# Optimization experiments

Hardware: AMD Instinct MI355X
Metric: run time of the kernel (lower is better)

Reference implementation:

```python
import jax, jax.numpy as jnp
import numpy as np

NEG = -9.0e15


def setup_inputs() -> dict:
    key = jax.random.key(0)
    k_x, k_w, k_e, k_b, k_m = jax.random.split(key, 5)
    B, N, C, F = 2048, 64, 256, 256
    x = jax.random.normal(k_x, (B, N, C), dtype=jnp.float32)
    W = jax.random.normal(k_w, (2, C, F), dtype=jnp.float32) * (1.414 / np.sqrt(C + F))
    # full logit tensor; only entries where mask holds are ever read (equivalent
    # to torch's flat `e` scattered into the nonzero positions of adj)
    e = jax.random.normal(k_e, (F, N, N), dtype=jnp.float32)
    bias = jax.random.normal(k_b, (F,), dtype=jnp.float32) * (1.0 / np.sqrt(C))
    # symmetric adjacency mask with self-loops, density ~0.3
    m = jax.random.bernoulli(k_m, 0.3, (N, N))
    mask = (m | m.T) | jnp.eye(N, dtype=bool)
    return {"x": x, "W": W, "e": e, "bias": bias, "mask": mask}


def reference(x, W, e, bias, mask):
    # x: [B,N,C], W: [2,C,F], e: [F,N,N], bias: [F], mask: [N,N] bool
    h0 = x @ W[0]                                   # [B,N,F] (self term)
    h1 = x @ W[1]                                   # [B,N,F] (neighbor term)
    logits = jnp.where(mask[None, :, :], e, NEG)    # [F,N,N]
    adj = jax.nn.softmax(logits, axis=2)            # per-channel row softmax
    N = mask.shape[0]
    eye = jnp.eye(N, dtype=bool)
    d = jnp.diagonal(adj, axis1=1, axis2=2)         # [F,N]  (adj * E diagonal)
    off = jnp.where(eye[None, :, :], 0.0, adj)      # [F,N,N] (adj * (1-E))
    # (adj*E) @ h0 reduces to per-node diagonal scaling; off-diag is a
    # per-channel NxN matmul batched over B.
    out = d.T[None, :, :] * h0 + jnp.einsum('fnm,bmf->bnf', off, h1)
    return out + bias[None, None, :]
```

## Files before the change

kernel.cpp:

```cpp
#include <hip/hip_runtime.h>
#include <hip/hip_bf16.h>


typedef __attribute__((ext_vector_type(8))) short  fragA;
typedef __attribute__((ext_vector_type(4))) float  f32x4;
typedef __attribute__((ext_vector_type(8))) unsigned short u16x8;
typedef __attribute__((ext_vector_type(4))) unsigned short u16x4;

constexpr long OFF_OFF = 0;
constexpr long OFF_WT  = 2l * 1024 * 1024;
constexpr long OFF_DS  = OFF_WT + 512l * 256 * 2;
constexpr long OFF_XB  = OFF_DS + 64l * 256 * 4;
constexpr long OFF_G0  = OFF_XB + 131072l * 256 * 2;
constexpr long OFF_H1T = OFF_G0 + 131072l * 256 * 2;
constexpr long WS_NEED = OFF_H1T + 131072l * 256 * 2;

static __device__ inline unsigned short f2bf(float f) {
  __hip_bfloat16 h = __float2bfloat16(f);
  return __builtin_bit_cast(unsigned short, h);
}
static __device__ inline float bf2f(unsigned short u) {
  unsigned int x = ((unsigned int)u) << 16;
  return __builtin_bit_cast(float, x);
}
static __device__ __forceinline__ void gl16(const void* g, void* l) {
  __builtin_amdgcn_global_load_lds(
      (const __attribute__((address_space(1))) unsigned int*)g,
      (__attribute__((address_space(3))) unsigned int*)l, 16, 0, 0);
}
static __device__ __forceinline__ f32x4 mfma16(fragA a, fragA b, f32x4 c) {
  return __builtin_amdgcn_mfma_f32_16x16x32_bf16(a, b, c, 0, 0, 0);
}

__global__ __launch_bounds__(256) void k_pre(const float* __restrict__ x,
                                             const float* __restrict__ e,
                                             const float* __restrict__ W,
                                             const unsigned char* __restrict__ mask,
                                             char* __restrict__ ws_b) {
  const int bid = blockIdx.x;
  const int tid = threadIdx.x;
  if (bid < 4096) {
    unsigned short* off = (unsigned short*)(ws_b + OFF_OFF);
    float* dscale = (float*)(ws_b + OFF_DS);
    const int lane = tid & 63;
    const int row  = bid * 4 + (tid >> 6);
    const int n = row & 63;
    bool is_u8 = __all(mask[lane * 65] != 0);
    bool mv;
    if (is_u8) mv = mask[n * 64 + lane] != 0;
    else       mv = ((const int*)mask)[n * 64 + lane] != 0;
    float v = mv ? e[(long)row * 64 + lane] : -1e30f;
    float mx = v;
#pragma unroll
    for (int s = 32; s; s >>= 1) mx = fmaxf(mx, __shfl_xor(mx, s));
    float ex = mv ? __expf(v - mx) : 0.f;
    float sm = ex;
#pragma unroll
    for (int s = 32; s; s >>= 1) sm += __shfl_xor(sm, s);
    float adj = ex / sm;
    const int f = row >> 6;
    if (lane == n) dscale[n * 256 + f] = adj;
    off[(long)row * 64 + lane] = f2bf(lane == n ? 0.f : adj);
  } else if (bid < 6144) {
    unsigned short* xb = (unsigned short*)(ws_b + OFF_XB);
    long i = ((long)(bid - 4096) * 256 + tid) * 8;
    const long stride = 2048l * 256 * 8;
    const long total = 131072l * 256;
    for (; i < total; i += stride) {
      float4 a = *(const float4*)(x + i);
      float4 b = *(const float4*)(x + i + 4);
      u16x8 p;
      p[0] = f2bf(a.x); p[1] = f2bf(a.y); p[2] = f2bf(a.z); p[3] = f2bf(a.w);
      p[4] = f2bf(b.x); p[5] = f2bf(b.y); p[6] = f2bf(b.z); p[7] = f2bf(b.w);
      *(u16x8*)(xb + i) = p;
    }
  } else {
    unsigned short* Wt = (unsigned short*)(ws_b + OFF_WT);
    __shared__ float t[64][65];
    const int b2 = bid - 6144;
    const int w = b2 >> 4, f0 = ((b2 >> 2) & 3) * 64, c0 = (b2 & 3) * 64;
    const int tr = tid >> 2, tc = (tid & 3) * 16;
    const float* src = W + ((long)(w * 256 + c0 + tr)) * 256 + f0 + tc;
#pragma unroll
    for (int i = 0; i < 16; i += 4) {
      float4 v = *(const float4*)(src + i);
      t[tr][tc + i] = v.x; t[tr][tc + i + 1] = v.y;
      t[tr][tc + i + 2] = v.z; t[tr][tc + i + 3] = v.w;
    }
    __syncthreads();
    u16x8 p0, p1;
#pragma unroll
    for (int i = 0; i < 8; i++)  p0[i] = f2bf(t[tc + i][tr]);
#pragma unroll
    for (int i = 0; i < 8; i++)  p1[i] = f2bf(t[tc + 8 + i][tr]);
    unsigned short* dst = Wt + ((long)(w * 256 + f0 + tr)) * 256 + c0 + tc;
    *(u16x8*)dst = p0;
    *(u16x8*)(dst + 8) = p1;
  }
}

__global__ __launch_bounds__(256) void k_gemm(char* __restrict__ ws_b) {
  const float* dscale = (const float*)(ws_b + OFF_DS);
  const char* xb_b = ws_b + OFF_XB;
  const char* wt_b = ws_b + OFF_WT;
  unsigned short* g0g = (unsigned short*)(ws_b + OFF_G0);
  unsigned short* h1t = (unsigned short*)(ws_b + OFF_H1T);

  __shared__ __align__(16) char arena[65536];

  const int tid = threadIdx.x;
  const int wid = tid >> 6, lane = tid & 63;
  const int lr = lane & 15, qu = lane >> 4;

  const int wg = blockIdx.x;
  const int xcd = wg & 7, s = wg >> 3;
  const int rg = xcd * 128 + (s >> 3);
  const int cg = s & 7;
  const int f0 = cg * 32;
  const long R0 = (long)rg * 128;

  {
    const int c  = tid >> 5;
    const int cb = (tid & 31) * 16;
    const int sw = cb ^ ((c & 7) << 4);
#pragma unroll
    for (int i = 0; i < 8; i++) {
      int col  = i * 8 + c;
      int wrow = (col < 32) ? (f0 + col) : (224 + f0 + col);
      gl16(wt_b + (long)wrow * 512 + sw, arena + i * 4096 + tid * 16);
    }
  }
  const int ar = tid >> 3;
  const int aswz = ((tid & 7) ^ (ar & 7)) << 4;
#pragma unroll
  for (int i = 0; i < 4; i++)
    gl16(xb_b + (R0 + i * 32 + ar) * 512 + aswz, arena + 32768 + i * 4096 + tid * 16);

  f32x4 acc[2][4] = {};
  const int arow0 = wid * 32;

  for (int ks = 0; ks < 4; ks++) {
    __syncthreads();
    if (ks < 3) {
      const char* gsrc = xb_b + (ks + 1) * 128;
      char* ldst = arena + 32768 + ((ks + 1) & 1) * 16384;
#pragma unroll
      for (int i = 0; i < 4; i++)
        gl16(gsrc + (R0 + i * 32 + ar) * 512 + aswz, ldst + i * 4096 + tid * 16);
    }
    const char* ab = arena + 32768 + (ks & 1) * 16384;
    fragA af[2][2], bfr[2][4];
#pragma unroll
    for (int kk = 0; kk < 2; kk++) {
#pragma unroll
      for (int i2 = 0; i2 < 2; i2++) {
        int r = arow0 + i2 * 16 + lr;
        af[kk][i2] = *(const fragA*)(ab + r * 128 +
                        ((kk * 64 + qu * 16) ^ ((lr & 7) << 4)));
      }
#pragma unroll
      for (int j = 0; j < 4; j++) {
        int cc = j * 16 + lr;
        bfr[kk][j] = *(const fragA*)(arena + cc * 512 +
                        ((ks * 128 + kk * 64 + qu * 16) ^ ((lr & 7) << 4)));
      }
    }
#pragma unroll
    for (int kk = 0; kk < 2; kk++)
#pragma unroll
      for (int i2 = 0; i2 < 2; i2++)
#pragma unroll
        for (int j = 0; j < 4; j++)
          acc[i2][j] = mfma16(af[kk][i2], bfr[kk][j], acc[i2][j]);
  }
  __syncthreads();

  unsigned short* Gs = (unsigned short*)(arena + 32768);
  unsigned short* Ts = (unsigned short*)(arena + 49152);
#pragma unroll
  for (int i2 = 0; i2 < 2; i2++) {
#pragma unroll
    for (int j = 0; j < 2; j++) {
      int f = f0 + j * 16 + lr;
#pragma unroll
      for (int r = 0; r < 4; r++) {
        int rloc = arow0 + i2 * 16 + qu * 4 + r;
        int n = rloc & 63;
        Gs[rloc * 40 + j * 16 + lr] = f2bf(dscale[n * 256 + f] * acc[i2][j][r]);
      }
    }
#pragma unroll
    for (int j = 2; j < 4; j++) {
      int fl = (j - 2) * 16 + lr;
      int rb = arow0 + i2 * 16 + qu * 4;
      u16x4 pk;
      pk[0] = f2bf(acc[i2][j][0]); pk[1] = f2bf(acc[i2][j][1]);
      pk[2] = f2bf(acc[i2][j][2]); pk[3] = f2bf(acc[i2][j][3]);
      *(u16x4*)(Ts + fl * 136 + rb) = pk;
    }
  }
  __syncthreads();

  {
    int row = tid >> 1, half = tid & 1;
    const unsigned short* sp = Gs + row * 40 + half * 16;
    unsigned short* dp = g0g + (R0 + row) * 256 + f0 + half * 16;
    *(u16x8*)dp = *(const u16x8*)sp;
    *(u16x8*)(dp + 8) = *(const u16x8*)(sp + 8);
  }
  {
    int f = tid >> 3, seg = tid & 7;
    const unsigned short* sp = Ts + f * 136 + seg * 16;
    unsigned short* dp = h1t + (long)(f0 + f) * 131072 + R0 + seg * 16;
    *(u16x8*)dp = *(const u16x8*)sp;
    *(u16x8*)(dp + 8) = *(const u16x8*)(sp + 8);
  }
}

__global__ __launch_bounds__(256) void k_eout(const float* __restrict__ bias,
                                              const char* __restrict__ ws_b,
                                              float* __restrict__ out) {
  const unsigned short* offp = (const unsigned short*)(ws_b + OFF_OFF);
  const unsigned short* h1t  = (const unsigned short*)(ws_b + OFF_H1T);
  const unsigned short* g0g  = (const unsigned short*)(ws_b + OFF_G0);

  __shared__ __align__(16) unsigned short Es[16 * 64 * 36];

  const int tid = threadIdx.x;
  const int wid = tid >> 6, lane = tid & 63;
  const int lr = lane & 15, qu = lane >> 4;

  const int wg = blockIdx.x;
  const int xcd = wg & 7, u = wg >> 3;
  const int bg = xcd * 16 + (u >> 3);
  const int fg = u & 7;
  const long B0 = (long)bg * 16;
  const int f0 = fg * 32;

#pragma unroll 2
  for (int q = 0; q < 8; q++) {
    const int fi = wid * 8 + q;
    const long fglob = f0 + fi;
    const unsigned short* hb_p = h1t + fglob * 131072 + (B0 + lr) * 64;
    const unsigned short* ob   = offp + fglob * 4096;
    fragA hb0 = *(const fragA*)(hb_p + qu * 8);
    fragA hb1 = *(const fragA*)(hb_p + 32 + qu * 8);
    f32x4 ea[4] = {};
#pragma unroll
    for (int ct = 0; ct < 4; ct++) {
      fragA o0 = *(const fragA*)(ob + (ct * 16 + lr) * 64 + qu * 8);
      fragA o1 = *(const fragA*)(ob + (ct * 16 + lr) * 64 + 32 + qu * 8);
      ea[ct] = mfma16(o0, hb0, ea[ct]);
      ea[ct] = mfma16(o1, hb1, ea[ct]);
    }
    const int fsw = fi ^ ((lr & 7) << 2);
#pragma unroll
    for (int ct = 0; ct < 4; ct++)
#pragma unroll
      for (int r = 0; r < 4; r++) {
        int n = ct * 16 + qu * 4 + r;
        Es[lr * 2304 + n * 36 + fsw] = f2bf(ea[ct][r]);
      }
  }
  __syncthreads();

  float4 bv[8];
#pragma unroll
  for (int k = 0; k < 8; k++) bv[k] = ((const float4*)(bias + f0))[k];
#pragma unroll
  for (int i = 0; i < 4; i++) {
    int rl = tid + 256 * i;
    int b = rl >> 6, n = rl & 63;
    long gRow = (B0 + b) * 64 + n;
    const unsigned short* gp = g0g + gRow * 256 + f0;
    u16x8 g[4];
#pragma unroll
    for (int k = 0; k < 4; k++) g[k] = ((const u16x8*)gp)[k];
    u16x4 ev[8];
#pragma unroll
    for (int gg = 0; gg < 8; gg++)
      ev[gg] = *(const u16x4*)&Es[b * 2304 + n * 36 + ((gg ^ (b & 7)) << 2)];
    float4* op = (float4*)(out + gRow * 256 + f0);
#pragma unroll
    for (int k = 0; k < 8; k++) {
      float4 ov;
      ov.x = bf2f(g[k >> 1][(k & 1) * 4 + 0]) + bf2f(ev[k][0]) + bv[k].x;
      ov.y = bf2f(g[k >> 1][(k & 1) * 4 + 1]) + bf2f(ev[k][1]) + bv[k].y;
      ov.z = bf2f(g[k >> 1][(k & 1) * 4 + 2]) + bf2f(ev[k][2]) + bv[k].z;
      ov.w = bf2f(g[k >> 1][(k & 1) * 4 + 3]) + bf2f(ev[k][3]) + bv[k].w;
      op[k] = ov;
    }
  }
}

extern "C" void kernel_launch(void* const* d_in, const int* in_sizes, int n_in,
                              void* d_out, int out_size, void* d_ws, size_t ws_size,
                              hipStream_t stream) {
  const float* x    = (const float*)d_in[0];
  const float* W    = (const float*)d_in[1];
  const float* e    = (const float*)d_in[2];
  const float* bias = (const float*)d_in[3];
  const unsigned char* mask = (const unsigned char*)d_in[4];
  float* out = (float*)d_out;
  char* ws = (char*)d_ws;
  if (ws_size < (size_t)WS_NEED) return;

  k_pre<<<6176, 256, 0, stream>>>(x, e, W, mask, ws);
  k_gemm<<<8192, 256, 0, stream>>>(ws);
  k_eout<<<1024, 256, 0, stream>>>(bias, ws, out);
}
```

Before: 239.6 us.

## Stream W tiles per k-step in gemm and halve eout channel tile

The gemm kernel no longer preloads the full 64x256 W slice into LDS. It double-buffers W chunks alongside the x chunks per k-step, which cuts LDS from 64KB to 48KB so more workgroups can be resident. The eout kernel now handles 16 channels per workgroup instead of 32 and launches twice as many blocks, halving its LDS staging buffer and changing the swizzle to match. The cost is more global loads of W, re-fetched per k-step, and more eout blocks, each reloading its offset matrices.

```diff
diff --git a/kernel.cpp b/kernel.cpp
--- a/kernel.cpp
+++ b/kernel.cpp
@@ -106,7 +106,7 @@
   unsigned short* g0g = (unsigned short*)(ws_b + OFF_G0);
   unsigned short* h1t = (unsigned short*)(ws_b + OFF_H1T);
 
-  __shared__ __align__(16) char arena[65536];
+  __shared__ __align__(16) char arena[49152];
 
   const int tid = threadIdx.x;
   const int wid = tid >> 6, lane = tid & 63;
@@ -119,22 +119,18 @@
   const int f0 = cg * 32;
   const long R0 = (long)rg * 128;
 
-  {
-    const int c  = tid >> 5;
-    const int cb = (tid & 31) * 16;
-    const int sw = cb ^ ((c & 7) << 4);
-#pragma unroll
-    for (int i = 0; i < 8; i++) {
-      int col  = i * 8 + c;
-      int wrow = (col < 32) ? (f0 + col) : (224 + f0 + col);
-      gl16(wt_b + (long)wrow * 512 + sw, arena + i * 4096 + tid * 16);
-    }
-  }
-  const int ar = tid >> 3;
-  const int aswz = ((tid & 7) ^ (ar & 7)) << 4;
+  const int ar   = tid >> 3;
+  const int swz  = (((tid & 7) ^ (ar & 7)) << 4);
+
+  const int bc0 = tid >> 3;
+  const int wrow0 = f0 + bc0;
+  const int wrow1 = 224 + f0 + (bc0 + 32);
+
 #pragma unroll
   for (int i = 0; i < 4; i++)
-    gl16(xb_b + (R0 + i * 32 + ar) * 512 + aswz, arena + 32768 + i * 4096 + tid * 16);
+    gl16(xb_b + (R0 + i * 32 + ar) * 512 + swz, arena + i * 4096 + tid * 16);
+  gl16(wt_b + (long)wrow0 * 512 + swz, arena + 32768 + tid * 16);
+  gl16(wt_b + (long)wrow1 * 512 + swz, arena + 32768 + 4096 + tid * 16);
 
   f32x4 acc[2][4] = {};
   const int arow0 = wid * 32;
@@ -142,13 +138,19 @@
   for (int ks = 0; ks < 4; ks++) {
     __syncthreads();
     if (ks < 3) {
-      const char* gsrc = xb_b + (ks + 1) * 128;
-      char* ldst = arena + 32768 + ((ks + 1) & 1) * 16384;
+      const int nb = (ks + 1) & 1;
+      const long ko = (ks + 1) * 128;
 #pragma unroll
       for (int i = 0; i < 4; i++)
-        gl16(gsrc + (R0 + i * 32 + ar) * 512 + aswz, ldst + i * 4096 + tid * 16);
-    }
-    const char* ab = arena + 32768 + (ks & 1) * 16384;
+        gl16(xb_b + (R0 + i * 32 + ar) * 512 + ko + swz,
+             arena + nb * 16384 + i * 4096 + tid * 16);
+      gl16(wt_b + (long)wrow0 * 512 + ko + swz,
+           arena + 32768 + nb * 8192 + tid * 16);
+      gl16(wt_b + (long)wrow1 * 512 + ko + swz,
+           arena + 32768 + nb * 8192 + 4096 + tid * 16);
+    }
+    const char* ab = arena + (ks & 1) * 16384;
+    const char* bb = arena + 32768 + (ks & 1) * 8192;
     fragA af[2][2], bfr[2][4];
 #pragma unroll
     for (int kk = 0; kk < 2; kk++) {
@@ -161,8 +163,8 @@
 #pragma unroll
       for (int j = 0; j < 4; j++) {
         int cc = j * 16 + lr;
-        bfr[kk][j] = *(const fragA*)(arena + cc * 512 +
-                        ((ks * 128 + kk * 64 + qu * 16) ^ ((lr & 7) << 4)));
+        bfr[kk][j] = *(const fragA*)(bb + cc * 128 +
+                        ((kk * 64 + qu * 16) ^ ((lr & 7) << 4)));
       }
     }
 #pragma unroll
@@ -175,8 +177,8 @@
   }
   __syncthreads();
 
-  unsigned short* Gs = (unsigned short*)(arena + 32768);
-  unsigned short* Ts = (unsigned short*)(arena + 49152);
+  unsigned short* Gs = (unsigned short*)(arena);
+  unsigned short* Ts = (unsigned short*)(arena + 16384);
 #pragma unroll
   for (int i2 = 0; i2 < 2; i2++) {
 #pragma unroll
@@ -224,7 +226,7 @@
   const unsigned short* h1t  = (const unsigned short*)(ws_b + OFF_H1T);
   const unsigned short* g0g  = (const unsigned short*)(ws_b + OFF_G0);
 
-  __shared__ __align__(16) unsigned short Es[16 * 64 * 36];
+  __shared__ __align__(16) unsigned short Es[16 * 64 * 18];
 
   const int tid = threadIdx.x;
   const int wid = tid >> 6, lane = tid & 63;
@@ -232,14 +234,14 @@
 
   const int wg = blockIdx.x;
   const int xcd = wg & 7, u = wg >> 3;
-  const int bg = xcd * 16 + (u >> 3);
-  const int fg = u & 7;
+  const int bg = xcd * 16 + (u >> 4);
+  const int fg = u & 15;
   const long B0 = (long)bg * 16;
-  const int f0 = fg * 32;
-
-#pragma unroll 2
-  for (int q = 0; q < 8; q++) {
-    const int fi = wid * 8 + q;
+  const int f0 = fg * 16;
+
+#pragma unroll
+  for (int q = 0; q < 4; q++) {
+    const int fi = wid * 4 + q;
     const long fglob = f0 + fi;
     const unsigned short* hb_p = h1t + fglob * 131072 + (B0 + lr) * 64;
     const unsigned short* ob   = offp + fglob * 4096;
@@ -253,41 +255,44 @@
       ea[ct] = mfma16(o0, hb0, ea[ct]);
       ea[ct] = mfma16(o1, hb1, ea[ct]);
     }
-    const int fsw = fi ^ ((lr & 7) << 2);
+    const int fsw = fi ^ ((lr & 3) << 2);
 #pragma unroll
     for (int ct = 0; ct < 4; ct++)
 #pragma unroll
       for (int r = 0; r < 4; r++) {
         int n = ct * 16 + qu * 4 + r;
-        Es[lr * 2304 + n * 36 + fsw] = f2bf(ea[ct][r]);
+        Es[lr * 1152 + n * 18 + fsw] = f2bf(ea[ct][r]);
       }
   }
   __syncthreads();
 
-  float4 bv[8];
-#pragma unroll
-  for (int k = 0; k < 8; k++) bv[k] = ((const float4*)(bias + f0))[k];
+  float4 bv[4];
+#pragma unroll
+  for (int k = 0; k < 4; k++) bv[k] = ((const float4*)(bias + f0))[k];
 #pragma unroll
   for (int i = 0; i < 4; i++) {
     int rl = tid + 256 * i;
     int b = rl >> 6, n = rl & 63;
     long gRow = (B0 + b) * 64 + n;
     const unsigned short* gp = g0g + gRow * 256 + f0;
-    u16x8 g[4];
-#pragma unroll
-    for (int k = 0; k < 4; k++) g[k] = ((const u16x8*)gp)[k];
-    u16x4 ev[8];
-#pragma unroll
-    for (int gg = 0; gg < 8; gg++)
-      ev[gg] = *(const u16x4*)&Es[b * 2304 + n * 36 + ((gg ^ (b & 7)) << 2)];
+    u16x8 gv0 = ((const u16x8*)gp)[0];
+    u16x8 gv1 = ((const u16x8*)gp)[1];
+    u16x4 ev[4];
+#pragma unroll
+    for (int gg = 0; gg < 4; gg++)
+      ev[gg] = *(const u16x4*)&Es[b * 1152 + n * 18 + ((gg << 2) ^ ((b & 3) << 2))];
     float4* op = (float4*)(out + gRow * 256 + f0);
 #pragma unroll
-    for (int k = 0; k < 8; k++) {
+    for (int k = 0; k < 4; k++) {
       float4 ov;
-      ov.x = bf2f(g[k >> 1][(k & 1) * 4 + 0]) + bf2f(ev[k][0]) + bv[k].x;
-      ov.y = bf2f(g[k >> 1][(k & 1) * 4 + 1]) + bf2f(ev[k][1]) + bv[k].y;
-      ov.z = bf2f(g[k >> 1][(k & 1) * 4 + 2]) + bf2f(ev[k][2]) + bv[k].z;
-      ov.w = bf2f(g[k >> 1][(k & 1) * 4 + 3]) + bf2f(ev[k][3]) + bv[k].w;
+      float g0e = bf2f(k < 2 ? gv0[(k & 1) * 4 + 0] : gv1[(k & 1) * 4 + 0]);
+      float g1e = bf2f(k < 2 ? gv0[(k & 1) * 4 + 1] : gv1[(k & 1) * 4 + 1]);
+      float g2e = bf2f(k < 2 ? gv0[(k & 1) * 4 + 2] : gv1[(k & 1) * 4 + 2]);
+      float g3e = bf2f(k < 2 ? gv0[(k & 1) * 4 + 3] : gv1[(k & 1) * 4 + 3]);
+      ov.x = g0e + bf2f(ev[k][0]) + bv[k].x;
+      ov.y = g1e + bf2f(ev[k][1]) + bv[k].y;
+      ov.z = g2e + bf2f(ev[k][2]) + bv[k].z;
+      ov.w = g3e + bf2f(ev[k][3]) + bv[k].w;
       op[k] = ov;
     }
   }
@@ -307,5 +312,5 @@
 
   k_pre<<<6176, 256, 0, stream>>>(x, e, W, mask, ws);
   k_gemm<<<8192, 256, 0, stream>>>(ws);
-  k_eout<<<1024, 256, 0, stream>>>(bias, ws, out);
-}
+  k_eout<<<2048, 256, 0, stream>>>(bias, ws, out);
+}
```

After: 227.0 us. -5.2%, faster.
